# Performance work log

Measured on AMD Instinct MI355X. Metric: run time of the kernel, lower is better.

## Reference

```python
import jax, jax.numpy as jnp
import numpy as np

NQ, NK, D = 256, 2048, 128

def setup_inputs() -> dict:
    key = jax.random.key(0)
    ks = jax.random.split(key, 12)
    s = lambda fan_in: 1.0 / np.sqrt(fan_in)
    inp = {
        "x": jax.random.normal(ks[0], (1, D, NQ), jnp.float32),
        "source": jax.random.normal(ks[1], (1, D, NK), jnp.float32),
        "dist": jax.random.normal(ks[2], (1, D, NQ * NK), jnp.float32),
        "mask": jax.random.randint(ks[3], (1, NQ, NK), 0, 2).astype(bool),
        # MLPAttention scoring MLP: Conv1d(384->128,k=1) + ReLU + Conv1d(128->1,k=1)
        "w1": jax.random.uniform(ks[4], (D, 3 * D), jnp.float32, -s(3 * D), s(3 * D)),
        "b1": jax.random.uniform(ks[5], (D,), jnp.float32, -s(3 * D), s(3 * D)),
        "w2": jax.random.uniform(ks[6], (1, D), jnp.float32, -s(D), s(D)),
        "b2": jax.random.uniform(ks[7], (1,), jnp.float32, -s(D), s(D)),
        # AttentionalPropagation MLP: Conv1d(256->256,k=1) + ReLU + Conv1d(256->128,k=1), last bias = 0
        "w3": jax.random.uniform(ks[8], (2 * D, 2 * D), jnp.float32, -s(2 * D), s(2 * D)),
        "b3": jax.random.uniform(ks[9], (2 * D,), jnp.float32, -s(2 * D), s(2 * D)),
        "w4": jax.random.uniform(ks[10], (D, 2 * D), jnp.float32, -s(2 * D), s(2 * D)),
        "b4": jnp.zeros((D,), jnp.float32),
    }
    return inp


def reference(x, source, dist, mask, w1, b1, w2, b2, w3, b3, w4, b4):
    b, d, nq = x.shape
    nk = source.shape[-1]
    # Conv1d(k=1) on concat(q_bcast, k_bcast, dist) == split-weight matmuls (same math, no giant concat)
    wq, wk, wd = w1[:, :d], w1[:, d:2 * d], w1[:, 2 * d:]
    qh = jnp.einsum('oc,bcn->bon', wq, x)                      # [b,d,nq]
    kh = jnp.einsum('oc,bcm->bom', wk, source)                 # [b,d,nk]
    dh = jnp.einsum('oc,bcnm->bonm', wd, dist.reshape(b, d, nq, nk))  # [b,d,nq,nk]
    h = jax.nn.relu(qh[:, :, :, None] + kh[:, :, None, :] + dh + b1[None, :, None, None])
    scores = jnp.einsum('c,bcnm->bnm', w2[0], h) + b2[0]       # [b,nq,nk]
    # boolean mask branch: scores + (min - 20) * (~mask)
    neg = jax.lax.stop_gradient(scores.min()) - 20.0
    scores = scores + neg * (~mask).astype(scores.dtype)
    prob = jax.nn.softmax(scores, axis=-1)
    message = jnp.einsum('bnm,bdm->bdn', prob, source)         # value == source
    # output MLP on concat([x, message], channel dim)
    cat = jnp.concatenate([x, message], axis=1)                # [b,2d,nq]
    hid = jax.nn.relu(jnp.einsum('oc,bcn->bon', w3, cat) + b3[None, :, None])
    out = jnp.einsum('oc,bcn->bon', w4, hid) + b4[None, :, None]
    return out, scores
```

## Files before the change

### kernel.cpp

```cpp
#include <hip/hip_runtime.h>
#include <hip/hip_bf16.h>

#define D_ 128
#define NQ_ 256
#define NK_ 2048
#define P_TOT (NQ_ * NK_)

typedef float f32x4 __attribute__((ext_vector_type(4)));
typedef short bf16x8 __attribute__((ext_vector_type(8)));

__device__ __forceinline__ unsigned short f2bf(float x) {
    union { float f; unsigned u; } v; v.f = x;
    unsigned r = v.u + 0x7FFFu + ((v.u >> 16) & 1u);
    return (unsigned short)(r >> 16);
}

__device__ __forceinline__ void gload16(const float* g, float* l) {
    __builtin_amdgcn_global_load_lds((const __attribute__((address_space(1))) void*)g,
                                     (__attribute__((address_space(3))) void*)l, 16, 0, 0);
}

__global__ __launch_bounds__(256) void k_prep(
    const float* __restrict__ w1, const float* __restrict__ x,
    const float* __restrict__ b1, const float* __restrict__ src,
    const float* __restrict__ w3, const float* __restrict__ b3,
    float* __restrict__ qb, float* __restrict__ kh, float* __restrict__ p1,
    unsigned* __restrict__ minw) {
    int b = blockIdx.x, t = threadIdx.x;
    if (b == 0 && t == 0) *minw = 0xFFFFFFFFu;
    if (b < 128) {
        int o = b, n = t;
        const float* wr = w1 + o * 384;
        float acc = b1[o];
#pragma unroll 4
        for (int c = 0; c < 128; ++c) acc = fmaf(wr[c], x[c * 256 + n], acc);
        qb[o * 256 + n] = acc;
    } else if (b < 1152) {
        int idx = (b - 128) * 256 + t;
        int o = idx >> 11, m = idx & 2047;
        const float* wr = w1 + o * 384 + 128;
        float acc = 0.f;
#pragma unroll 4
        for (int c = 0; c < 128; ++c) acc = fmaf(wr[c], src[c * 2048 + m], acc);
        kh[o * 2048 + m] = acc;
    } else {
        int o = b - 1152, n = t;
        const float* wr = w3 + o * 256;
        float acc = b3[o];
#pragma unroll 4
        for (int c = 0; c < 128; ++c) acc = fmaf(wr[c], x[c * 256 + n], acc);
        p1[o * 256 + n] = acc;
    }
}

__global__ __launch_bounds__(512, 2) void k_scores(
    const float* __restrict__ dist, const float* __restrict__ w1,
    const float* __restrict__ qb, const float* __restrict__ kh,
    const float* __restrict__ w2, const float* __restrict__ b2,
    float* __restrict__ scores, unsigned* __restrict__ minw) {
    __shared__ __align__(16) float lds[34176];
    float* buf0 = lds;
    float* buf1 = lds + 8192;
    unsigned short* khT = (unsigned short*)(lds + 16384);
    float* qbT = lds + 33024;
    float* w2l = lds + 34048;

    const int tid = threadIdx.x;
    const int l = tid & 63, wid = tid >> 6;
    const int lg = l >> 4, c16 = l & 15;
    const int mb = blockIdx.x & 7, nb = blockIdx.x >> 3;
    const int m0 = mb * 256, n0 = nb * 8;

    {
        bf16x8* ldsA = (bf16x8*)lds;
#pragma unroll
        for (int i = 0; i < 4; ++i) {
            int s = tid + i * 512;
            int o = s >> 4, oct = s & 15;
            const float* gp = w1 + o * 384 + 256 + oct * 8;
            float4 f0 = *(const float4*)gp;
            float4 f1 = *(const float4*)(gp + 4);
            union { bf16x8 v; unsigned short u[8]; } pk;
            pk.u[0] = f2bf(f0.x); pk.u[1] = f2bf(f0.y); pk.u[2] = f2bf(f0.z); pk.u[3] = f2bf(f0.w);
            pk.u[4] = f2bf(f1.x); pk.u[5] = f2bf(f1.y); pk.u[6] = f2bf(f1.z); pk.u[7] = f2bf(f1.w);
            int mt = o >> 4, kt = oct >> 2;
            int lane2 = ((oct & 3) << 4) | (o & 15);
            ldsA[(mt * 4 + kt) * 64 + lane2] = pk.v;
        }
    }
#pragma unroll
    for (int jj = 0; jj < 16; ++jj) {
        int e = tid + jj * 512;
        int o = e >> 6, mq = e & 63;
        float4 f = *(const float4*)&kh[o * 2048 + m0 + mq * 4];
        khT[(mq * 4 + 0) * 130 + o] = f2bf(f.x);
        khT[(mq * 4 + 1) * 130 + o] = f2bf(f.y);
        khT[(mq * 4 + 2) * 130 + o] = f2bf(f.z);
        khT[(mq * 4 + 3) * 130 + o] = f2bf(f.w);
    }
#pragma unroll
    for (int jj = 0; jj < 2; ++jj) {
        int e = tid + jj * 512;
        int o = e >> 3, nl2 = e & 7;
        qbT[nl2 * 128 + o] = qb[o * 256 + n0 + nl2];
    }
    if (tid < 128) w2l[tid] = w2[tid];
    __syncthreads();

    bf16x8 A[8][4];
    {
        bf16x8* ldsA = (bf16x8*)lds;
#pragma unroll
        for (int mt = 0; mt < 8; ++mt)
#pragma unroll
            for (int kt = 0; kt < 4; ++kt)
                A[mt][kt] = ldsA[(mt * 4 + kt) * 64 + l];
    }
    __syncthreads();

    f32x4 acc[2][8];
#pragma unroll
    for (int s = 0; s < 2; ++s)
#pragma unroll
        for (int mt = 0; mt < 8; ++mt) acc[s][mt] = (f32x4){0.f, 0.f, 0.f, 0.f};

    const float b2v = b2[0];
    float runmin = 1e30f;

    auto issueT = [&](int n_l, int cq, float* buf) {
        const float* basep = dist + (size_t)(n0 + n_l) * 2048 + (size_t)m0;
#pragma unroll
        for (int j = 0; j < 4; ++j) {
            int row = wid * 4 + j;
            int x = ((row >> 3) & 1) << 2;
            gload16(basep + (size_t)(cq * 32 + row) * (size_t)P_TOT + ((l ^ x) << 2),
                    buf + row * 256);
        }
    };

    auto epi = [&](int nl) {
        const float* qr = qbT + nl * 128;
        float sc2[2];
#pragma unroll
        for (int s = 0; s < 2; ++s) {
            const unsigned short* khr = khT + (wid * 32 + s * 16 + c16) * 130;
            float sp = 0.f;
#pragma unroll
            for (int mt = 0; mt < 8; ++mt) {
                int o = mt * 16 + lg * 4;
                unsigned k01 = *(const unsigned*)(khr + o);
                unsigned k23 = *(const unsigned*)(khr + o + 2);
                float kh0 = __uint_as_float(k01 << 16);
                float kh1 = __uint_as_float(k01 & 0xffff0000u);
                float kh2 = __uint_as_float(k23 << 16);
                float kh3 = __uint_as_float(k23 & 0xffff0000u);
                float4 qv = *(const float4*)(qr + o);
                float4 wv = *(const float4*)(w2l + o);
                float t0 = fmaxf(acc[s][mt][0] + qv.x + kh0, 0.f);
                float t1 = fmaxf(acc[s][mt][1] + qv.y + kh1, 0.f);
                float t2 = fmaxf(acc[s][mt][2] + qv.z + kh2, 0.f);
                float t3 = fmaxf(acc[s][mt][3] + qv.w + kh3, 0.f);
                sp = fmaf(wv.x, t0, sp); sp = fmaf(wv.y, t1, sp);
                sp = fmaf(wv.z, t2, sp); sp = fmaf(wv.w, t3, sp);
                acc[s][mt] = (f32x4){0.f, 0.f, 0.f, 0.f};
            }
            sp += __shfl_xor(sp, 16);
            sp += __shfl_xor(sp, 32);
            sc2[s] = sp + b2v;
        }
        float wv = (l < 16) ? sc2[0] : sc2[1];
        if (l < 32) scores[(size_t)(n0 + nl) * 2048 + (size_t)(m0 + wid * 32) + l] = wv;
        float mn = fminf(sc2[0], sc2[1]);
        mn = fminf(mn, __shfl_xor(mn, 1));
        mn = fminf(mn, __shfl_xor(mn, 2));
        mn = fminf(mn, __shfl_xor(mn, 4));
        mn = fminf(mn, __shfl_xor(mn, 8));
        runmin = fminf(runmin, mn);
    };

    issueT(0, 0, buf0);
    issueT(0, 1, buf1);

#define STEP(CQ, NL, DO_ISSUE, LAST)                                             \
    {                                                                            \
        float* cur = ((CQ) & 1) ? buf1 : buf0;                                   \
        if (LAST) { asm volatile("s_waitcnt vmcnt(0)" ::: "memory"); }           \
        else      { asm volatile("s_waitcnt vmcnt(4)" ::: "memory"); }           \
        __builtin_amdgcn_sched_barrier(0);                                       \
        __builtin_amdgcn_s_barrier();                                            \
        _Pragma("unroll")                                                        \
        for (int s = 0; s < 2; ++s) {                                            \
            const int grpx = (wid * 8 + s * 4 + (c16 >> 2)) ^ ((lg & 1) << 2);   \
            const float* rp = cur + lg * 2048 + grpx * 4 + (c16 & 3);            \
            float tv[8];                                                         \
            _Pragma("unroll")                                                    \
            for (int b = 0; b < 8; ++b) tv[b] = rp[b * 256];                     \
            union { unsigned d[4]; bf16x8 v; } bb;                               \
            _Pragma("unroll")                                                    \
            for (int i = 0; i < 4; ++i) {                                        \
                unsigned r0 = __float_as_uint(tv[2 * i])     + 0x8000u;          \
                unsigned r1 = __float_as_uint(tv[2 * i + 1]) + 0x8000u;          \
                bb.d[i] = __builtin_amdgcn_perm(r1, r0, 0x07060302u);            \
            }                                                                    \
            _Pragma("unroll")                                                    \
            for (int mt = 0; mt < 8; ++mt)                                       \
                acc[s][mt] = __builtin_amdgcn_mfma_f32_16x16x32_bf16(            \
                    A[mt][(CQ)], bb.v, acc[s][mt], 0, 0, 0);                     \
        }                                                                        \
        if ((CQ) == 3) epi(NL);                                                  \
        __builtin_amdgcn_s_barrier();                                            \
        if (DO_ISSUE) issueT((NL) + ((CQ) >= 2 ? 1 : 0), ((CQ) + 2) & 3, cur);   \
    }

    for (int nl = 0; nl < 7; ++nl) {
        STEP(0, nl, true, false)
        STEP(1, nl, true, false)
        STEP(2, nl, true, false)
        STEP(3, nl, true, false)
    }
    STEP(0, 7, true,  false)
    STEP(1, 7, true,  false)
    STEP(2, 7, false, false)
    STEP(3, 7, false, true)
#undef STEP

    union { float f; unsigned u; } e; e.f = runmin;
    unsigned key = (e.u & 0x80000000u) ? ~e.u : (e.u | 0x80000000u);
    if (l == 0) atomicMin(minw, key);
}

__global__ __launch_bounds__(256) void k_tail(
    float* __restrict__ scores, const int* __restrict__ mask,
    const float* __restrict__ src, const unsigned* __restrict__ minw,
    const float* __restrict__ w3, const float* __restrict__ w4,
    const float* __restrict__ b4, const float* __restrict__ p1,
    float* __restrict__ out) {
    __shared__ float sc[2][2048];
    __shared__ float red[2][8];
    __shared__ float msgl[2][128];
    __shared__ float hidl[2][256];
    const int t = threadIdx.x, l = t & 63, wv = t >> 6;
    const int n0 = blockIdx.x * 2;

    unsigned key = *minw;
    union { float f; unsigned u; } d;
    d.u = (key & 0x80000000u) ? (key ^ 0x80000000u) : ~key;
    const float neg = d.f - 20.f;

#pragma unroll
    for (int nn = 0; nn < 2; ++nn) {
        int n = n0 + nn;
        float lmax = -1e30f;
#pragma unroll
        for (int i = 0; i < 8; ++i) {
            int m = t + i * 256;
            float v = scores[n * 2048 + m];
            if (!mask[n * 2048 + m]) v += neg;
            scores[n * 2048 + m] = v;
            sc[nn][m] = v;
            lmax = fmaxf(lmax, v);
        }
#pragma unroll
        for (int off = 1; off < 64; off <<= 1) lmax = fmaxf(lmax, __shfl_xor(lmax, off));
        if (l == 0) red[nn][wv] = lmax;
    }
    __syncthreads();
    float smax[2], lsum[2] = {0.f, 0.f};
#pragma unroll
    for (int nn = 0; nn < 2; ++nn)
        smax[nn] = fmaxf(fmaxf(red[nn][0], red[nn][1]), fmaxf(red[nn][2], red[nn][3]));
#pragma unroll
    for (int nn = 0; nn < 2; ++nn) {
#pragma unroll
        for (int i = 0; i < 8; ++i) {
            int m = t + i * 256;
            float e = __expf(sc[nn][m] - smax[nn]);
            sc[nn][m] = e;
            lsum[nn] += e;
        }
#pragma unroll
        for (int off = 1; off < 64; off <<= 1) lsum[nn] += __shfl_xor(lsum[nn], off);
        if (l == 0) red[nn][4 + wv] = lsum[nn];
    }
    __syncthreads();
    const float rinv0 = 1.f / (red[0][4] + red[0][5] + red[0][6] + red[0][7]);
    const float rinv1 = 1.f / (red[1][4] + red[1][5] + red[1][6] + red[1][7]);

    for (int dd = 0; dd < 32; ++dd) {
        int dch = wv * 32 + dd;
        const float* sr = src + dch * 2048;
        float pa = 0.f, pb = 0.f;
#pragma unroll
        for (int j = 0; j < 32; ++j) {
            int mm = l + j * 64;
            float s = sr[mm];
            pa = fmaf(sc[0][mm], s, pa);
            pb = fmaf(sc[1][mm], s, pb);
        }
#pragma unroll
        for (int off = 1; off < 64; off <<= 1) {
            pa += __shfl_xor(pa, off);
            pb += __shfl_xor(pb, off);
        }
        if (l == 0) { msgl[0][dch] = pa * rinv0; msgl[1][dch] = pb * rinv1; }
    }
    __syncthreads();

    {
        int o = t;
        const float* wr = w3 + o * 256 + 128;
        float a0 = p1[o * 256 + n0];
        float a1 = p1[o * 256 + n0 + 1];
#pragma unroll
        for (int c = 0; c < 128; c += 4) {
            float4 w4v = *(const float4*)(wr + c);
            a0 = fmaf(w4v.x, msgl[0][c], a0);   a1 = fmaf(w4v.x, msgl[1][c], a1);
            a0 = fmaf(w4v.y, msgl[0][c + 1], a0); a1 = fmaf(w4v.y, msgl[1][c + 1], a1);
            a0 = fmaf(w4v.z, msgl[0][c + 2], a0); a1 = fmaf(w4v.z, msgl[1][c + 2], a1);
            a0 = fmaf(w4v.w, msgl[0][c + 3], a0); a1 = fmaf(w4v.w, msgl[1][c + 3], a1);
        }
        hidl[0][o] = fmaxf(a0, 0.f);
        hidl[1][o] = fmaxf(a1, 0.f);
    }
    __syncthreads();

    {
        int o = t & 127, nn = t >> 7;
        const float* wr = w4 + o * 256;
        const float* hr = hidl[nn];
        float acc = b4[o];
#pragma unroll
        for (int c = 0; c < 256; c += 4) {
            float4 w4v = *(const float4*)(wr + c);
            acc = fmaf(w4v.x, hr[c], acc);
            acc = fmaf(w4v.y, hr[c + 1], acc);
            acc = fmaf(w4v.z, hr[c + 2], acc);
            acc = fmaf(w4v.w, hr[c + 3], acc);
        }
        out[o * 256 + n0 + nn] = acc;
    }
}

extern "C" void kernel_launch(void* const* d_in, const int* in_sizes, int n_in,
                              void* d_out, int out_size, void* d_ws, size_t ws_size,
                              hipStream_t stream) {
    const float* x      = (const float*)d_in[0];
    const float* source = (const float*)d_in[1];
    const float* dist   = (const float*)d_in[2];
    const int*   mask   = (const int*)d_in[3];
    const float* w1     = (const float*)d_in[4];
    const float* b1     = (const float*)d_in[5];
    const float* w2     = (const float*)d_in[6];
    const float* b2     = (const float*)d_in[7];
    const float* w3     = (const float*)d_in[8];
    const float* b3     = (const float*)d_in[9];
    const float* w4     = (const float*)d_in[10];
    const float* b4     = (const float*)d_in[11];

    float* outp    = (float*)d_out;
    float* scoresp = outp + 32768;

    float* ws   = (float*)d_ws;
    float* qb   = ws;
    float* kh   = ws + 32768;
    float* p1   = ws + 294912;
    unsigned* minw = (unsigned*)(ws + 360448);

    k_prep<<<1408, 256, 0, stream>>>(w1, x, b1, source, w3, b3, qb, kh, p1, minw);
    k_scores<<<256, 512, 0, stream>>>(dist, w1, qb, kh, w2, b2, scoresp, minw);
    k_tail<<<128, 256, 0, stream>>>(scoresp, mask, source, minw, w3, w4, b4, p1, outp);
}
```

Measured before the change: 135.8 us.

## Deepen dist prefetch to four LDS buffers and keep kh slice in registers

Moves the per-thread kh values from an LDS transposed tile into packed bf16 registers loaded straight from global memory. The freed LDS is used to grow the dist staging ring from two buffers to four. Prefetch now runs three stages ahead, with the vmcnt waits adjusted to match. This targets memory latency stalls in the scores kernel, at the cost of 32 more VGPRs per thread under a 512-thread, 2-block launch bound, which risks spilling or lower occupancy.

Result: slower. 203.8 us (+50.1%).

```diff
diff --git a/kernel.cpp b/kernel.cpp
--- a/kernel.cpp
+++ b/kernel.cpp
@@ -19,6 +19,9 @@
     __builtin_amdgcn_global_load_lds((const __attribute__((address_space(1))) void*)g,
                                      (__attribute__((address_space(3))) void*)l, 16, 0, 0);
 }
+
+#define WAITVM_(n) asm volatile("s_waitcnt vmcnt(" #n ")" ::: "memory")
+#define WAITVM(n) WAITVM_(n)
 
 __global__ __launch_bounds__(256) void k_prep(
     const float* __restrict__ w1, const float* __restrict__ x,
@@ -58,12 +61,10 @@
     const float* __restrict__ qb, const float* __restrict__ kh,
     const float* __restrict__ w2, const float* __restrict__ b2,
     float* __restrict__ scores, unsigned* __restrict__ minw) {
-    __shared__ __align__(16) float lds[34176];
-    float* buf0 = lds;
-    float* buf1 = lds + 8192;
-    unsigned short* khT = (unsigned short*)(lds + 16384);
-    float* qbT = lds + 33024;
-    float* w2l = lds + 34048;
+    __shared__ __align__(16) float lds[33920];
+    float* bufs = lds;
+    float* qbT  = lds + 32768;
+    float* w2l  = lds + 33792;
 
     const int tid = threadIdx.x;
     const int l = tid & 63, wid = tid >> 6;
@@ -89,16 +90,6 @@
         }
     }
 #pragma unroll
-    for (int jj = 0; jj < 16; ++jj) {
-        int e = tid + jj * 512;
-        int o = e >> 6, mq = e & 63;
-        float4 f = *(const float4*)&kh[o * 2048 + m0 + mq * 4];
-        khT[(mq * 4 + 0) * 130 + o] = f2bf(f.x);
-        khT[(mq * 4 + 1) * 130 + o] = f2bf(f.y);
-        khT[(mq * 4 + 2) * 130 + o] = f2bf(f.z);
-        khT[(mq * 4 + 3) * 130 + o] = f2bf(f.w);
-    }
-#pragma unroll
     for (int jj = 0; jj < 2; ++jj) {
         int e = tid + jj * 512;
         int o = e >> 3, nl2 = e & 7;
@@ -116,7 +107,25 @@
             for (int kt = 0; kt < 4; ++kt)
                 A[mt][kt] = ldsA[(mt * 4 + kt) * 64 + l];
     }
-    __syncthreads();
+
+    unsigned khp[2][16];
+#pragma unroll
+    for (int s = 0; s < 2; ++s) {
+        const float* kp = kh + (size_t)(m0 + wid * 32 + s * 16 + c16);
+#pragma unroll
+        for (int mt = 0; mt < 8; ++mt) {
+            int o = mt * 16 + lg * 4;
+            float a0 = kp[(size_t)o * 2048];
+            float a1 = kp[(size_t)(o + 1) * 2048];
+            float a2 = kp[(size_t)(o + 2) * 2048];
+            float a3 = kp[(size_t)(o + 3) * 2048];
+            khp[s][mt * 2]     = (unsigned)f2bf(a0) | ((unsigned)f2bf(a1) << 16);
+            khp[s][mt * 2 + 1] = (unsigned)f2bf(a2) | ((unsigned)f2bf(a3) << 16);
+        }
+    }
+    __syncthreads();
+    WAITVM(0);
+    __builtin_amdgcn_sched_barrier(0);
 
     f32x4 acc[2][8];
 #pragma unroll
@@ -127,7 +136,9 @@
     const float b2v = b2[0];
     float runmin = 1e30f;
 
-    auto issueT = [&](int n_l, int cq, float* buf) {
+    auto issueT = [&](int t) {
+        int n_l = t >> 2, cq = t & 3;
+        float* buf = bufs + (size_t)(t & 3) * 8192;
         const float* basep = dist + (size_t)(n0 + n_l) * 2048 + (size_t)m0;
 #pragma unroll
         for (int j = 0; j < 4; ++j) {
@@ -143,13 +154,12 @@
         float sc2[2];
 #pragma unroll
         for (int s = 0; s < 2; ++s) {
-            const unsigned short* khr = khT + (wid * 32 + s * 16 + c16) * 130;
             float sp = 0.f;
 #pragma unroll
             for (int mt = 0; mt < 8; ++mt) {
                 int o = mt * 16 + lg * 4;
-                unsigned k01 = *(const unsigned*)(khr + o);
-                unsigned k23 = *(const unsigned*)(khr + o + 2);
+                unsigned k01 = khp[s][mt * 2];
+                unsigned k23 = khp[s][mt * 2 + 1];
                 float kh0 = __uint_as_float(k01 << 16);
                 float kh1 = __uint_as_float(k01 & 0xffff0000u);
                 float kh2 = __uint_as_float(k23 << 16);
@@ -178,14 +188,12 @@
         runmin = fminf(runmin, mn);
     };
 
-    issueT(0, 0, buf0);
-    issueT(0, 1, buf1);
-
-#define STEP(CQ, NL, DO_ISSUE, LAST)                                             \
+    issueT(0); issueT(1); issueT(2); issueT(3);
+
+#define STEP(CQ, NL, DO_ISSUE, VM)                                               \
     {                                                                            \
-        float* cur = ((CQ) & 1) ? buf1 : buf0;                                   \
-        if (LAST) { asm volatile("s_waitcnt vmcnt(0)" ::: "memory"); }           \
-        else      { asm volatile("s_waitcnt vmcnt(4)" ::: "memory"); }           \
+        float* cur = bufs + (CQ) * 8192;                                         \
+        WAITVM(VM);                                                              \
         __builtin_amdgcn_sched_barrier(0);                                       \
         __builtin_amdgcn_s_barrier();                                            \
         _Pragma("unroll")                                                        \
@@ -209,19 +217,19 @@
         }                                                                        \
         if ((CQ) == 3) epi(NL);                                                  \
         __builtin_amdgcn_s_barrier();                                            \
-        if (DO_ISSUE) issueT((NL) + ((CQ) >= 2 ? 1 : 0), ((CQ) + 2) & 3, cur);   \
+        if (DO_ISSUE) issueT((NL) * 4 + (CQ) + 4);                               \
     }
 
     for (int nl = 0; nl < 7; ++nl) {
-        STEP(0, nl, true, false)
-        STEP(1, nl, true, false)
-        STEP(2, nl, true, false)
-        STEP(3, nl, true, false)
-    }
-    STEP(0, 7, true,  false)
-    STEP(1, 7, true,  false)
-    STEP(2, 7, false, false)
-    STEP(3, 7, false, true)
+        STEP(0, nl, true, 12)
+        STEP(1, nl, true, 12)
+        STEP(2, nl, true, 12)
+        STEP(3, nl, true, 12)
+    }
+    STEP(0, 7, false, 12)
+    STEP(1, 7, false, 8)
+    STEP(2, 7, false, 4)
+    STEP(3, 7, false, 0)
 #undef STEP
 
     union { float f; unsigned u; } e; e.f = runmin;
@@ -314,7 +322,7 @@
 #pragma unroll
         for (int c = 0; c < 128; c += 4) {
             float4 w4v = *(const float4*)(wr + c);
-            a0 = fmaf(w4v.x, msgl[0][c], a0);   a1 = fmaf(w4v.x, msgl[1][c], a1);
+            a0 = fmaf(w4v.x, msgl[0][c], a0);     a1 = fmaf(w4v.x, msgl[1][c], a1);
             a0 = fmaf(w4v.y, msgl[0][c + 1], a0); a1 = fmaf(w4v.y, msgl[1][c + 1], a1);
             a0 = fmaf(w4v.z, msgl[0][c + 2], a0); a1 = fmaf(w4v.z, msgl[1][c + 2], a1);
             a0 = fmaf(w4v.w, msgl[0][c + 3], a0); a1 = fmaf(w4v.w, msgl[1][c + 3], a1);
```
